# Performance work log

Hardware: AMD Instinct MI355X
Metric: run time of the kernel (lower is better)

## Reference

```python
import jax, jax.numpy as jnp
from jax import lax
import numpy as np

# CenterNet decode config
B, C, H, W = 16, 80, 128, 128  # batch, classes, feature-map H/W (512 input / down_ratio 4)
K = 100                        # top-K detections per image
DOWN = 4.0                     # down_ratio: feature-map coords -> input-image coords


def setup_inputs() -> dict:
    key = jax.random.key(0)
    k1, k2, k3 = jax.random.split(key, 3)
    return {
        "output_heatmap": jax.random.normal(k1, (B, C, H, W), dtype=jnp.float32),
        "output_bbox": jax.random.uniform(k2, (B, 2, H, W), dtype=jnp.float32) * 32.0,  # wh head
        "output_offset": jax.random.uniform(k3, (B, 2, H, W), dtype=jnp.float32),       # sub-pixel offset head
        "image_id": jnp.arange(B, dtype=jnp.int32),
    }


def reference(output_heatmap, output_bbox, output_offset, image_id):
    # 1) peak scores
    hm = jax.nn.sigmoid(output_heatmap)  # [B,C,H,W]
    # 2) 3x3 maxpool NMS: keep only local maxima
    hmax = lax.reduce_window(hm, -jnp.inf, lax.max,
                             window_dimensions=(1, 1, 3, 3),
                             window_strides=(1, 1, 1, 1),
                             padding='SAME')
    hm = jnp.where(hmax == hm, hm, jnp.zeros((), hm.dtype))
    # 3) per-image top-K over all classes and positions
    scores, inds = lax.top_k(hm.reshape(B, C * H * W), K)  # [B,K]
    cls = (inds // (H * W)).astype(jnp.float32)             # [B,K]
    sp = inds % (H * W)                                     # spatial index in [0, H*W)
    ys = (sp // W).astype(jnp.float32)
    xs = (sp % W).astype(jnp.float32)
    # 4) sparse gather of offset and wh at the K peak locations
    off = jnp.take_along_axis(output_offset.reshape(B, 2, H * W), sp[:, None, :], axis=2)  # [B,2,K]
    wh = jnp.take_along_axis(output_bbox.reshape(B, 2, H * W), sp[:, None, :], axis=2)     # [B,2,K]
    cx = xs + off[:, 0]
    cy = ys + off[:, 1]
    w = wh[:, 0]
    h = wh[:, 1]
    # 5) decode to corner boxes in input-image coordinates
    boxes = jnp.stack([cx - w / 2, cy - h / 2, cx + w / 2, cy + h / 2], axis=-1) * DOWN  # [B,K,4]
    img = jnp.broadcast_to(image_id[:, None].astype(jnp.float32), (B, K))
    # detections: [image_id, x1, y1, x2, y2, score, class] -> [B,K,7]
    det = jnp.concatenate([img[..., None], boxes, scores[..., None], cls[..., None]], axis=-1)
    return det
```

## Files before the change

### kernel.cpp

```cpp
#include <hip/hip_runtime.h>

#define BB 16
#define CC 80
#define HWs 16384
#define KK 100
#define NBIN 2048
#define NSLOT 320
#define BCAP 576
#define SBCAP 32

#define OFF_BHIST 0
#define OFF_CUT   131072
#define OFF_PBCNT 131136
#define OFF_PSCNT 151616
#define OFF_REC   172096
#define OFF_SURV  11968576

__device__ __forceinline__ unsigned okey(float f) {
    unsigned u = __float_as_uint(f);
    return (u & 0x80000000u) ? ~u : (u | 0x80000000u);
}

__global__ __launch_bounds__(256) void zero_hist_kernel(int4* __restrict__ bhist) {
    int i = blockIdx.x * 256 + threadIdx.x;
    if (i < BB * NBIN / 4) bhist[i] = make_int4(0, 0, 0, 0);
}

__global__ __launch_bounds__(256) void nms_kernel(const float* __restrict__ hm,
                                                  unsigned* __restrict__ rec,
                                                  int* __restrict__ pbcnt,
                                                  int* __restrict__ bhist) {
    __shared__ int hist[NBIN];
    __shared__ int wbase[4];
    const int blk = blockIdx.x;
    const int plane = blk >> 2;
    const int band = blk & 3;
    const int b = plane / CC;
    const int c = plane - b * CC;
    const int slot = (c << 2) | band;
    const int t = threadIdx.x;
    const int lane = t & 63;
    const int wid = t >> 6;
    const int sx = t & 31;
    const int x0 = sx << 2;
    const int y0 = (band << 5) + ((t >> 5) << 2);
    const float4* __restrict__ src4 =
        reinterpret_cast<const float4*>(hm + (size_t)plane * HWs);

    for (int i = t; i < NBIN; i += 256) hist[i] = 0;
    __syncthreads();

    float4 v[6];
#pragma unroll
    for (int r = 0; r < 6; ++r) {
        int rr = y0 - 1 + r;
        rr = rr < 0 ? 0 : (rr > 127 ? 127 : rr);
        v[r] = src4[(rr << 5) + sx];
    }

    auto hmax3 = [&](const float4& a) -> float4 {
        float vm1 = __shfl_up(a.w, 1, 32);
        float vp4 = __shfl_down(a.x, 1, 32);
        if (sx == 0) vm1 = a.x;
        if (sx == 31) vp4 = a.w;
        float4 h;
        h.x = fmaxf(fmaxf(vm1, a.x), a.y);
        h.y = fmaxf(fmaxf(a.x, a.y), a.z);
        h.z = fmaxf(fmaxf(a.y, a.z), a.w);
        h.w = fmaxf(fmaxf(a.z, a.w), vp4);
        return h;
    };

    unsigned pmask = 0;
    float4 hm1 = hmax3(v[0]);
    float4 h0  = hmax3(v[1]);
#pragma unroll
    for (int r = 0; r < 4; ++r) {
        float4 hp1 = hmax3(v[r + 2]);
        if (v[r + 1].x >= fmaxf(fmaxf(hm1.x, h0.x), hp1.x)) pmask |= 1u << (r * 4 + 0);
        if (v[r + 1].y >= fmaxf(fmaxf(hm1.y, h0.y), hp1.y)) pmask |= 1u << (r * 4 + 1);
        if (v[r + 1].z >= fmaxf(fmaxf(hm1.z, h0.z), hp1.z)) pmask |= 1u << (r * 4 + 2);
        if (v[r + 1].w >= fmaxf(fmaxf(hm1.w, h0.w), hp1.w)) pmask |= 1u << (r * 4 + 3);
        hm1 = h0; h0 = hp1;
    }

    int cntp = __popc(pmask);
    int sc = cntp;
#pragma unroll
    for (int off = 1; off < 64; off <<= 1) {
        int n = __shfl_up(sc, off, 64);
        if (lane >= off) sc += n;
    }
    if (lane == 63) wbase[wid] = sc;
    __syncthreads();
    int wexcl = 0;
#pragma unroll
    for (int i = 0; i < 4; ++i) if (i < wid) wexcl += wbase[i];
    int w = wexcl + sc - cntp;

    unsigned* __restrict__ rb = rec + ((size_t)b * NSLOT + slot) * BCAP;
#pragma unroll
    for (int r = 0; r < 4; ++r) {
        float vv0 = v[r + 1].x, vv1 = v[r + 1].y, vv2 = v[r + 1].z, vv3 = v[r + 1].w;
#pragma unroll
        for (int j = 0; j < 4; ++j) {
            if (pmask & (1u << (r * 4 + j))) {
                float lv = (j == 0) ? vv0 : (j == 1) ? vv1 : (j == 2) ? vv2 : vv3;
                unsigned bin = okey(lv) >> 21;
                atomicAdd(&hist[bin], 1);
                unsigned idx = ((unsigned)c << 14) | ((unsigned)(y0 + r) << 7)
                             | (unsigned)(x0 + j);
                if (w < BCAP) rb[w] = (bin << 21) | idx;
                ++w;
            }
        }
    }
    if (t == 0) {
        int tot = wbase[0] + wbase[1] + wbase[2] + wbase[3];
        pbcnt[b * NSLOT + slot] = tot > BCAP ? BCAP : tot;
    }

    __syncthreads();
    for (int i = t; i < NBIN; i += 256) {
        int hv = hist[i];
        if (hv) atomicAdd(&bhist[b * NBIN + i], hv);
    }
}

__global__ __launch_bounds__(256) void cut_kernel(const int* __restrict__ bhist,
                                                  int* __restrict__ cut) {
    __shared__ int csum[256];
    __shared__ int s_cut;
    const int b = blockIdx.x;
    const int t = threadIdx.x;

    int h[8]; int chunk = 0;
#pragma unroll
    for (int j = 0; j < 8; ++j) {
        h[j] = bhist[b * NBIN + (t << 3) + j];
        chunk += h[j];
    }
    csum[t] = chunk;
    if (t == 0) s_cut = 0;
    __syncthreads();
    for (int off = 1; off < 256; off <<= 1) {
        int v = (t + off < 256) ? csum[t + off] : 0;
        __syncthreads();
        csum[t] += v;
        __syncthreads();
    }
    if (csum[0] > KK) {
        int running = (t < 255) ? csum[t + 1] : 0;
        if (csum[t] >= KK && running < KK) {
            for (int j = 7; j >= 0; --j) {
                running += h[j];
                if (running >= KK) { s_cut = (t << 3) + j; break; }
            }
        }
    }
    __syncthreads();
    if (t == 0) cut[b] = s_cut;
}

__global__ __launch_bounds__(256) void filter_kernel(const unsigned* __restrict__ rec,
                                                     const int* __restrict__ pbcnt,
                                                     const int* __restrict__ cut,
                                                     unsigned* __restrict__ surv,
                                                     int* __restrict__ pscnt) {
    __shared__ int s_n;
    const int bx = blockIdx.x;
    const int b = bx / NSLOT;
    const int t = threadIdx.x;
    if (t == 0) s_n = 0;
    __syncthreads();

    int n = pbcnt[bx]; if (n > BCAP) n = BCAP;
    const int cutb = cut[b];
    const unsigned* __restrict__ rb = rec + (size_t)bx * BCAP;
    unsigned* __restrict__ sb = surv + (size_t)bx * SBCAP;
    for (int i = t; i < n; i += 256) {
        unsigned rv = rb[i];
        if ((int)(rv >> 21) >= cutb) {
            int sl = atomicAdd(&s_n, 1);
            if (sl < SBCAP) sb[sl] = rv & 0x1FFFFFu;
        }
    }
    __syncthreads();
    if (t == 0) pscnt[bx] = s_n > SBCAP ? SBCAP : s_n;
}

__global__ __launch_bounds__(256) void topk_kernel(const unsigned* __restrict__ surv,
                                                   const int* __restrict__ pscnt,
                                                   const float* __restrict__ hm,
                                                   const float* __restrict__ bbox,
                                                   const float* __restrict__ offs,
                                                   const int* __restrict__ image_id,
                                                   float* __restrict__ out) {
    __shared__ int lcnt[NSLOT];
    __shared__ unsigned uidx[2048];
    __shared__ unsigned long long list[2048];
    __shared__ int s_n;
    const int b = blockIdx.x;
    const int t = threadIdx.x;
    const float* __restrict__ hb = hm + (size_t)b * CC * HWs;

    for (int s = t; s < NSLOT; s += 256) lcnt[s] = pscnt[b * NSLOT + s];
    if (t == 0) s_n = 0;
    __syncthreads();

    for (int s = t; s < NSLOT; s += 256) {
        int cs = lcnt[s]; if (cs > SBCAP) cs = SBCAP;
        if (cs) {
            int base = atomicAdd(&s_n, cs);
            const unsigned* __restrict__ sb = surv + ((size_t)b * NSLOT + s) * SBCAP;
            for (int k = 0; k < cs; ++k)
                if (base + k < 2048) uidx[base + k] = sb[k];
        }
    }
    __syncthreads();
    int n = s_n; if (n > 2048) n = 2048;

    for (int i = t; i < n; i += 256) {
        unsigned idx = uidx[i];
        float lv = hb[idx];
        float s = 1.0f / (1.0f + expf(-lv));
        list[i] = ((unsigned long long)__float_as_uint(s) << 32) | (unsigned)(~idx);
    }
    int P = 128;
    while (P < n) P <<= 1;
    for (int i = n + t; i < P; i += 256) list[i] = 0ull;
    __syncthreads();

    for (int ksz = 2; ksz <= P; ksz <<= 1) {
        for (int j = ksz >> 1; j > 0; j >>= 1) {
            for (int i = t; i < P; i += 256) {
                int ixj = i ^ j;
                if (ixj > i) {
                    unsigned long long a = list[i], bb2 = list[ixj];
                    bool desc = ((i & ksz) == 0);
                    if (desc ? (a < bb2) : (a > bb2)) { list[i] = bb2; list[ixj] = a; }
                }
            }
            __syncthreads();
        }
    }

    if (t < KK) {
        float s = 0.0f; unsigned idx = 0;
        if (t < n) {
            unsigned long long cv = list[t];
            s = __uint_as_float((unsigned)(cv >> 32));
            idx = ~(unsigned)(cv & 0xFFFFFFFFu) & 0x1FFFFFu;
        }
        unsigned sp = idx & (HWs - 1);
        float cls = (float)(idx >> 14);
        float ysf = (float)(sp >> 7);
        float xsf = (float)(sp & 127);
        const float* __restrict__ ob  = offs + (size_t)b * 2 * HWs;
        const float* __restrict__ bbx = bbox + (size_t)b * 2 * HWs;
        float cx = xsf + ob[sp];
        float cy = ysf + ob[HWs + sp];
        float w = bbx[sp];
        float h = bbx[HWs + sp];
        float* row = out + ((size_t)b * KK + t) * 7;
        row[0] = (float)image_id[b];
        row[1] = (cx - w * 0.5f) * 4.0f;
        row[2] = (cy - h * 0.5f) * 4.0f;
        row[3] = (cx + w * 0.5f) * 4.0f;
        row[4] = (cy + h * 0.5f) * 4.0f;
        row[5] = s;
        row[6] = cls;
    }
}

extern "C" void kernel_launch(void* const* d_in, const int* in_sizes, int n_in,
                              void* d_out, int out_size, void* d_ws, size_t ws_size,
                              hipStream_t stream) {
    const float* hm      = (const float*)d_in[0];
    const float* bbox    = (const float*)d_in[1];
    const float* offset  = (const float*)d_in[2];
    const int*   img_id  = (const int*)d_in[3];
    float* out = (float*)d_out;

    char* ws = (char*)d_ws;
    int*      bhist = (int*)(ws + OFF_BHIST);
    int*      cut   = (int*)(ws + OFF_CUT);
    int*      pbcnt = (int*)(ws + OFF_PBCNT);
    int*      pscnt = (int*)(ws + OFF_PSCNT);
    unsigned* rec   = (unsigned*)(ws + OFF_REC);
    unsigned* surv  = (unsigned*)(ws + OFF_SURV);

    zero_hist_kernel<<<32, 256, 0, stream>>>((int4*)bhist);
    nms_kernel<<<BB * CC * 4, 256, 0, stream>>>(hm, rec, pbcnt, bhist);
    cut_kernel<<<BB, 256, 0, stream>>>(bhist, cut);
    filter_kernel<<<BB * NSLOT, 256, 0, stream>>>(rec, pbcnt, cut, surv, pscnt);
    topk_kernel<<<BB, 256, 0, stream>>>(surv, pscnt, hm, bbox, offset, img_id, out);
}
```

Baseline: 65.45 us.

## Process whole heatmap plane per NMS block instead of four bands

```diff
diff --git a/kernel.cpp b/kernel.cpp
--- a/kernel.cpp
+++ b/kernel.cpp
@@ -5,16 +5,15 @@
 #define HWs 16384
 #define KK 100
 #define NBIN 2048
-#define NSLOT 320
-#define BCAP 576
-#define SBCAP 32
+#define BCAP 2304
+#define SBCAP 128
 
 #define OFF_BHIST 0
 #define OFF_CUT   131072
 #define OFF_PBCNT 131136
-#define OFF_PSCNT 151616
-#define OFF_REC   172096
-#define OFF_SURV  11968576
+#define OFF_PSCNT 136256
+#define OFF_REC   141376
+#define OFF_SURV  11937856
 
 __device__ __forceinline__ unsigned okey(float f) {
     unsigned u = __float_as_uint(f);
@@ -32,31 +31,20 @@
                                                   int* __restrict__ bhist) {
     __shared__ int hist[NBIN];
     __shared__ int wbase[4];
-    const int blk = blockIdx.x;
-    const int plane = blk >> 2;
-    const int band = blk & 3;
+    const int plane = blockIdx.x;
     const int b = plane / CC;
     const int c = plane - b * CC;
-    const int slot = (c << 2) | band;
     const int t = threadIdx.x;
     const int lane = t & 63;
     const int wid = t >> 6;
     const int sx = t & 31;
     const int x0 = sx << 2;
-    const int y0 = (band << 5) + ((t >> 5) << 2);
+    const int band0 = (t >> 5) << 4;
     const float4* __restrict__ src4 =
         reinterpret_cast<const float4*>(hm + (size_t)plane * HWs);
 
     for (int i = t; i < NBIN; i += 256) hist[i] = 0;
     __syncthreads();
-
-    float4 v[6];
-#pragma unroll
-    for (int r = 0; r < 6; ++r) {
-        int rr = y0 - 1 + r;
-        rr = rr < 0 ? 0 : (rr > 127 ? 127 : rr);
-        v[r] = src4[(rr << 5) + sx];
-    }
 
     auto hmax3 = [&](const float4& a) -> float4 {
         float vm1 = __shfl_up(a.w, 1, 32);
@@ -71,56 +59,71 @@
         return h;
     };
 
-    unsigned pmask = 0;
-    float4 hm1 = hmax3(v[0]);
-    float4 h0  = hmax3(v[1]);
-#pragma unroll
-    for (int r = 0; r < 4; ++r) {
-        float4 hp1 = hmax3(v[r + 2]);
-        if (v[r + 1].x >= fmaxf(fmaxf(hm1.x, h0.x), hp1.x)) pmask |= 1u << (r * 4 + 0);
-        if (v[r + 1].y >= fmaxf(fmaxf(hm1.y, h0.y), hp1.y)) pmask |= 1u << (r * 4 + 1);
-        if (v[r + 1].z >= fmaxf(fmaxf(hm1.z, h0.z), hp1.z)) pmask |= 1u << (r * 4 + 2);
-        if (v[r + 1].w >= fmaxf(fmaxf(hm1.w, h0.w), hp1.w)) pmask |= 1u << (r * 4 + 3);
-        hm1 = h0; h0 = hp1;
-    }
-
-    int cntp = __popc(pmask);
-    int sc = cntp;
-#pragma unroll
-    for (int off = 1; off < 64; off <<= 1) {
-        int n = __shfl_up(sc, off, 64);
-        if (lane >= off) sc += n;
-    }
-    if (lane == 63) wbase[wid] = sc;
-    __syncthreads();
-    int wexcl = 0;
-#pragma unroll
-    for (int i = 0; i < 4; ++i) if (i < wid) wexcl += wbase[i];
-    int w = wexcl + sc - cntp;
-
-    unsigned* __restrict__ rb = rec + ((size_t)b * NSLOT + slot) * BCAP;
-#pragma unroll
-    for (int r = 0; r < 4; ++r) {
-        float vv0 = v[r + 1].x, vv1 = v[r + 1].y, vv2 = v[r + 1].z, vv3 = v[r + 1].w;
-#pragma unroll
-        for (int j = 0; j < 4; ++j) {
-            if (pmask & (1u << (r * 4 + j))) {
-                float lv = (j == 0) ? vv0 : (j == 1) ? vv1 : (j == 2) ? vv2 : vv3;
-                unsigned bin = okey(lv) >> 21;
-                atomicAdd(&hist[bin], 1);
-                unsigned idx = ((unsigned)c << 14) | ((unsigned)(y0 + r) << 7)
-                             | (unsigned)(x0 + j);
-                if (w < BCAP) rb[w] = (bin << 21) | idx;
-                ++w;
+    unsigned* __restrict__ rb = rec + (size_t)plane * BCAP;
+    int rbase = 0;
+
+#pragma unroll
+    for (int chunk = 0; chunk < 4; ++chunk) {
+        const int y0 = band0 + (chunk << 2);
+
+        float4 v[6];
+#pragma unroll
+        for (int r = 0; r < 6; ++r) {
+            int rr = y0 - 1 + r;
+            rr = rr < 0 ? 0 : (rr > 127 ? 127 : rr);
+            v[r] = src4[(rr << 5) + sx];
+        }
+
+        unsigned pmask = 0;
+        float4 hm1 = hmax3(v[0]);
+        float4 h0  = hmax3(v[1]);
+#pragma unroll
+        for (int r = 0; r < 4; ++r) {
+            float4 hp1 = hmax3(v[r + 2]);
+            if (v[r + 1].x >= fmaxf(fmaxf(hm1.x, h0.x), hp1.x)) pmask |= 1u << (r * 4 + 0);
+            if (v[r + 1].y >= fmaxf(fmaxf(hm1.y, h0.y), hp1.y)) pmask |= 1u << (r * 4 + 1);
+            if (v[r + 1].z >= fmaxf(fmaxf(hm1.z, h0.z), hp1.z)) pmask |= 1u << (r * 4 + 2);
+            if (v[r + 1].w >= fmaxf(fmaxf(hm1.w, h0.w), hp1.w)) pmask |= 1u << (r * 4 + 3);
+            hm1 = h0; h0 = hp1;
+        }
+
+        int cntp = __popc(pmask);
+        int sc = cntp;
+#pragma unroll
+        for (int off = 1; off < 64; off <<= 1) {
+            int n = __shfl_up(sc, off, 64);
+            if (lane >= off) sc += n;
+        }
+        if (lane == 63) wbase[wid] = sc;
+        __syncthreads();
+        int wexcl = 0;
+#pragma unroll
+        for (int i = 0; i < 4; ++i) if (i < wid) wexcl += wbase[i];
+        const int blocktot = wbase[0] + wbase[1] + wbase[2] + wbase[3];
+        int w = rbase + wexcl + sc - cntp;
+
+#pragma unroll
+        for (int r = 0; r < 4; ++r) {
+            float vv0 = v[r + 1].x, vv1 = v[r + 1].y, vv2 = v[r + 1].z, vv3 = v[r + 1].w;
+#pragma unroll
+            for (int j = 0; j < 4; ++j) {
+                if (pmask & (1u << (r * 4 + j))) {
+                    float lv = (j == 0) ? vv0 : (j == 1) ? vv1 : (j == 2) ? vv2 : vv3;
+                    unsigned bin = okey(lv) >> 21;
+                    atomicAdd(&hist[bin], 1);
+                    unsigned idx = ((unsigned)c << 14) | ((unsigned)(y0 + r) << 7)
+                                 | (unsigned)(x0 + j);
+                    if (w < BCAP) rb[w] = (bin << 21) | idx;
+                    ++w;
+                }
             }
         }
-    }
-    if (t == 0) {
-        int tot = wbase[0] + wbase[1] + wbase[2] + wbase[3];
-        pbcnt[b * NSLOT + slot] = tot > BCAP ? BCAP : tot;
-    }
-
-    __syncthreads();
+        __syncthreads();
+        rbase += blocktot;
+    }
+
+    if (t == 0) pbcnt[plane] = rbase > BCAP ? BCAP : rbase;
+
     for (int i = t; i < NBIN; i += 256) {
         int hv = hist[i];
         if (hv) atomicAdd(&bhist[b * NBIN + i], hv);
@@ -169,7 +172,7 @@
                                                      int* __restrict__ pscnt) {
     __shared__ int s_n;
     const int bx = blockIdx.x;
-    const int b = bx / NSLOT;
+    const int b = bx / CC;
     const int t = threadIdx.x;
     if (t == 0) s_n = 0;
     __syncthreads();
@@ -196,7 +199,7 @@
                                                    const float* __restrict__ offs,
                                                    const int* __restrict__ image_id,
                                                    float* __restrict__ out) {
-    __shared__ int lcnt[NSLOT];
+    __shared__ int lcnt[CC];
     __shared__ unsigned uidx[2048];
     __shared__ unsigned long long list[2048];
     __shared__ int s_n;
@@ -204,15 +207,15 @@
     const int t = threadIdx.x;
     const float* __restrict__ hb = hm + (size_t)b * CC * HWs;
 
-    for (int s = t; s < NSLOT; s += 256) lcnt[s] = pscnt[b * NSLOT + s];
+    if (t < CC) lcnt[t] = pscnt[b * CC + t];
     if (t == 0) s_n = 0;
     __syncthreads();
 
-    for (int s = t; s < NSLOT; s += 256) {
+    for (int s = t; s < CC; s += 256) {
         int cs = lcnt[s]; if (cs > SBCAP) cs = SBCAP;
         if (cs) {
             int base = atomicAdd(&s_n, cs);
-            const unsigned* __restrict__ sb = surv + ((size_t)b * NSLOT + s) * SBCAP;
+            const unsigned* __restrict__ sb = surv + ((size_t)b * CC + s) * SBCAP;
             for (int k = 0; k < cs; ++k)
                 if (base + k < 2048) uidx[base + k] = sb[k];
         }
@@ -291,8 +294,8 @@
     unsigned* surv  = (unsigned*)(ws + OFF_SURV);
 
     zero_hist_kernel<<<32, 256, 0, stream>>>((int4*)bhist);
-    nms_kernel<<<BB * CC * 4, 256, 0, stream>>>(hm, rec, pbcnt, bhist);
+    nms_kernel<<<BB * CC, 256, 0, stream>>>(hm, rec, pbcnt, bhist);
     cut_kernel<<<BB, 256, 0, stream>>>(bhist, cut);
-    filter_kernel<<<BB * NSLOT, 256, 0, stream>>>(rec, pbcnt, cut, surv, pscnt);
+    filter_kernel<<<BB * CC, 256, 0, stream>>>(rec, pbcnt, cut, surv, pscnt);
     topk_kernel<<<BB, 256, 0, stream>>>(surv, pscnt, hm, bbox, offset, img_id, out);
 }
```

New measurement: 62.33 us. -4.8%, faster.
